# Optimization experiments

Measured on AMD Instinct MI355X. Metric: run time of the kernel, lower is better.

Reference implementation:

```python
import jax, jax.numpy as jnp
import numpy as np

B, T, C = 2, 2048, 2048
H = 16
D = C // H  # head_dim = 128


def rotate_half(x):
    x1, x2 = jnp.split(x, 2, axis=-1)
    return jnp.concatenate([-x2, x1], axis=-1)


def apply_rotary(q, k, cos, sin):
    # q,k: (B,H,T,D); cos,sin: (T,D/2)
    cos2 = jnp.concatenate([cos, cos], axis=-1)[None, None]  # (1,1,T,D)
    sin2 = jnp.concatenate([sin, sin], axis=-1)[None, None]
    return q * cos2 + rotate_half(q) * sin2, k * cos2 + rotate_half(k) * sin2


def setup_inputs() -> dict:
    key = jax.random.key(0)
    k1, k2, k3, k4 = jax.random.split(key, 4)
    x = jax.random.normal(k1, (B, T, C), dtype=jnp.float32)
    w_qkv = jax.random.normal(k2, (C, 3 * C), dtype=jnp.float32) * (C ** -0.5)
    w_out = jax.random.normal(k3, (C, C), dtype=jnp.float32) * (C ** -0.5)
    pos = jnp.arange(T, dtype=jnp.float32)[:, None]
    inv_freq = 1.0 / (10000.0 ** (jnp.arange(0, D, 2, dtype=jnp.float32) / D))  # (D/2,)
    ang = pos * inv_freq[None, :]  # (T, D/2)
    return {"x": x, "w_qkv": w_qkv, "w_out": w_out,
            "cos": jnp.cos(ang), "sin": jnp.sin(ang)}


def reference(x, w_qkv, w_out, cos, sin):
    b, t, c = x.shape
    qkv = x @ w_qkv  # (B,T,3C)
    qkv = qkv.reshape(b, t, 3, H, D)
    q, k, v = qkv[:, :, 0], qkv[:, :, 1], qkv[:, :, 2]  # (B,T,H,D)
    q = q.transpose(0, 2, 1, 3)  # (B,H,T,D)
    k = k.transpose(0, 2, 1, 3)
    v = v.transpose(0, 2, 1, 3)
    q, k = apply_rotary(q, k, cos, sin)
    scale = 1.0 / jnp.sqrt(jnp.asarray(D, dtype=x.dtype))
    scores = jnp.einsum('bhqd,bhkd->bhqk', q, k) * scale  # (B,H,T,T)
    causal = jnp.tril(jnp.ones((t, t), dtype=bool))
    scores = jnp.where(causal[None, None], scores, jnp.asarray(-jnp.inf, dtype=scores.dtype))
    attn = jax.nn.softmax(scores, axis=-1)
    out = jnp.einsum('bhqk,bhkd->bhqd', attn, v)  # (B,H,T,D)
    out = out.transpose(0, 2, 1, 3).reshape(b, t, c)
    return out @ w_out
```

## Files before the change

kernel.cpp:

```cpp
#include <hip/hip_runtime.h>


typedef __attribute__((ext_vector_type(8))) short short8;
typedef __attribute__((ext_vector_type(4))) float floatx4;
typedef __attribute__((ext_vector_type(4))) unsigned int uint4v;

#define MFMA16(a, b, c) __builtin_amdgcn_mfma_f32_16x16x32_bf16(a, b, c, 0, 0, 0)

__device__ inline unsigned short f2bf(float f) {
    union { float f; unsigned int i; } v; v.f = f;
    unsigned int r = v.i + 0x7fff + ((v.i >> 16) & 1);
    return (unsigned short)(r >> 16);
}

__device__ inline void gl2lds16(const unsigned short* g, unsigned short* l) {
    __builtin_amdgcn_global_load_lds(
        (const __attribute__((address_space(1))) unsigned int*)g,
        (__attribute__((address_space(3))) unsigned int*)l, 16, 0, 0);
}

__device__ __forceinline__ void bar_lds_only() {
    asm volatile("s_waitcnt lgkmcnt(0)" ::: "memory");
    __builtin_amdgcn_sched_barrier(0);
    __builtin_amdgcn_s_barrier();
    __builtin_amdgcn_sched_barrier(0);
}

__global__ __launch_bounds__(256) void cvt_k(const float* __restrict__ in,
                                             unsigned short* __restrict__ out, int n) {
    int i = (blockIdx.x * 256 + threadIdx.x) * 8;
    if (i + 7 < n) {
        float4 v0 = *(const float4*)(&in[i]);
        float4 v1 = *(const float4*)(&in[i + 4]);
        ushort4 o0, o1;
        o0.x = f2bf(v0.x); o0.y = f2bf(v0.y); o0.z = f2bf(v0.z); o0.w = f2bf(v0.w);
        o1.x = f2bf(v1.x); o1.y = f2bf(v1.y); o1.z = f2bf(v1.z); o1.w = f2bf(v1.w);
        *(ushort4*)(&out[i])     = o0;
        *(ushort4*)(&out[i + 4]) = o1;
    } else {
        for (int j = i; j < n; j++) out[j] = f2bf(in[j]);
    }
}

__global__ __launch_bounds__(256) void transpose_f2b_k(const float* __restrict__ in,
                                                       unsigned short* __restrict__ out,
                                                       int R, int Cc) {
    __shared__ unsigned short tile[32][33];
    int ct = blockIdx.x * 32;
    int rt = blockIdx.y * 32;
    int tx = threadIdx.x & 31;
    int ty = threadIdx.x >> 5;
#pragma unroll
    for (int i = 0; i < 32; i += 8)
        tile[ty + i][tx] = f2bf(in[(size_t)(rt + ty + i) * Cc + ct + tx]);
    __syncthreads();
#pragma unroll
    for (int i = 0; i < 32; i += 8)
        out[(size_t)(ct + ty + i) * R + rt + tx] = tile[tx][ty + i];
}

__global__ __launch_bounds__(256) void transpose_v_k(const unsigned short* __restrict__ qkv,
                                                     unsigned short* __restrict__ VT) {
    __shared__ unsigned short tile[32][33];
    int t0 = blockIdx.x * 32;
    int d0 = blockIdx.y * 32;
    int bh = blockIdx.z;
    int b = bh >> 4, h = bh & 15;
    int tx = threadIdx.x & 31;
    int ty = threadIdx.x >> 5;
#pragma unroll
    for (int i = 0; i < 32; i += 8)
        tile[ty + i][tx] =
            qkv[((size_t)(b * 2048 + t0 + ty + i) * 3 + 2) * 2048 + h * 128 + d0 + tx];
    __syncthreads();
#pragma unroll
    for (int i = 0; i < 32; i += 8)
        VT[((size_t)bh * 128 + d0 + ty + i) * 2048 + t0 + tx] = tile[tx][ty + i];
}

__global__ __launch_bounds__(256) void rotary_k(unsigned short* qkv,
                                                const float* __restrict__ cosT,
                                                const float* __restrict__ sinT) {
    int idx = blockIdx.x * 256 + threadIdx.x;
    int d    = idx & 63;
    int h    = (idx >> 6) & 15;
    int part = (idx >> 10) & 1;
    int t    = (idx >> 11) & 2047;
    int b    = idx >> 22;
    size_t base = ((size_t)(b * 2048 + t) * 3 + part) * 2048 + h * 128;
    float c = cosT[t * 64 + d];
    float s = sinT[t * 64 + d];
    union { unsigned int i; float f; } u1, u2;
    u1.i = ((unsigned int)qkv[base + d]) << 16;
    u2.i = ((unsigned int)qkv[base + d + 64]) << 16;
    float x1 = u1.f, x2 = u2.f;
    qkv[base + d]      = f2bf(x1 * c - x2 * s);
    qkv[base + d + 64] = f2bf(x2 * c + x1 * s);
}

template <bool OUTF32>
__global__ __launch_bounds__(256) void gemm_bt(const unsigned short* __restrict__ A, long lda,
                                               const unsigned short* __restrict__ Bt,
                                               void* __restrict__ Co, long ldc,
                                               int M, int N, int K) {
    __shared__ unsigned short a_lds[128 * 32];
    __shared__ unsigned short b_lds[128 * 32];
    int m0 = blockIdx.y * 128, n0 = blockIdx.x * 128;
    int tid = threadIdx.x;
    int lane = tid & 63, w = tid >> 6;
    int wm = (w >> 1) * 64, wn = (w & 1) * 64;
    int lr = lane & 15, quad = lane >> 4, lk = quad * 8;

    floatx4 acc[4][4];
    floatx4 zero4 = {0.f, 0.f, 0.f, 0.f};
#pragma unroll
    for (int i = 0; i < 4; i++)
#pragma unroll
        for (int j = 0; j < 4; j++) acc[i][j] = zero4;

    for (int k0 = 0; k0 < K; k0 += 32) {
#pragma unroll
        for (int i = 0; i < 2; i++) {
            int c = w * 128 + i * 64 + lane;
            int row = c >> 2, seg = (c & 3) * 8;
            gl2lds16(&A[(size_t)(m0 + row) * lda + k0 + seg], &a_lds[c * 8]);
            gl2lds16(&Bt[(size_t)(n0 + row) * K + k0 + seg], &b_lds[c * 8]);
        }
        __syncthreads();
        short8 af[4], bfr[4];
#pragma unroll
        for (int i = 0; i < 4; i++)
            af[i] = *(const short8*)(&a_lds[(wm + i * 16 + lr) * 32 + lk]);
#pragma unroll
        for (int j = 0; j < 4; j++)
            bfr[j] = *(const short8*)(&b_lds[(wn + j * 16 + lr) * 32 + lk]);
#pragma unroll
        for (int i = 0; i < 4; i++)
#pragma unroll
            for (int j = 0; j < 4; j++)
                acc[i][j] = MFMA16(af[i], bfr[j], acc[i][j]);
        __syncthreads();
    }
#pragma unroll
    for (int i = 0; i < 4; i++)
#pragma unroll
        for (int j = 0; j < 4; j++)
#pragma unroll
            for (int r = 0; r < 4; r++) {
                int row = m0 + wm + i * 16 + quad * 4 + r;
                int col = n0 + wn + j * 16 + lr;
                if (OUTF32)
                    ((float*)Co)[(size_t)row * ldc + col] = acc[i][j][r];
                else
                    ((unsigned short*)Co)[(size_t)row * ldc + col] = f2bf(acc[i][j][r]);
            }
}

__device__ __forceinline__ void attn_core(const short8 (&qf)[4], floatx4 (&o_acc)[8],
                                          float (&m_i)[4], float (&l_i)[4],
                                          const unsigned short* kb_lds,
                                          const unsigned short* vb_lds,
                                          unsigned short* p_w,
                                          int qrow0, int tk0, int lr, int quad, int lk) {
    floatx4 zero4 = {0.f, 0.f, 0.f, 0.f};
    const float scale = 0.08838834764831845f;

    floatx4 s[4];
#pragma unroll
    for (int n = 0; n < 4; n++) {
        s[n] = zero4;
#pragma unroll
        for (int c = 0; c < 4; c++) {
            short8 kb = *(const short8*)(
                &kb_lds[(n * 16 + lr) * 128 + (((c * 4 + quad) ^ lr) * 8)]);
            s[n] = MFMA16(qf[c], kb, s[n]);
        }
    }

    float rmax[4];
#pragma unroll
    for (int r = 0; r < 4; r++) {
        int tqr = qrow0 + quad * 4 + r;
        float mx = -1e30f;
#pragma unroll
        for (int n = 0; n < 4; n++) {
            int tk = tk0 + n * 16 + lr;
            float sv = s[n][r] * scale;
            sv = (tk > tqr) ? -1e30f : sv;
            s[n][r] = sv;
            mx = fmaxf(mx, sv);
        }
        rmax[r] = mx;
    }
#pragma unroll
    for (int off = 1; off < 16; off <<= 1)
#pragma unroll
        for (int r = 0; r < 4; r++)
            rmax[r] = fmaxf(rmax[r], __shfl_xor(rmax[r], off, 64));

    float alpha[4], rsum[4];
#pragma unroll
    for (int r = 0; r < 4; r++) {
        float mn = fmaxf(m_i[r], rmax[r]);
        alpha[r] = __expf(m_i[r] - mn);
        m_i[r] = mn;
        rsum[r] = 0.f;
    }
#pragma unroll
    for (int n = 0; n < 4; n++)
#pragma unroll
        for (int r = 0; r < 4; r++) {
            float p = __expf(s[n][r] - m_i[r]);
            rsum[r] += p;
            p_w[(quad * 4 + r) * 72 + n * 16 + lr] = f2bf(p);
        }
#pragma unroll
    for (int off = 1; off < 16; off <<= 1)
#pragma unroll
        for (int r = 0; r < 4; r++)
            rsum[r] += __shfl_xor(rsum[r], off, 64);
#pragma unroll
    for (int r = 0; r < 4; r++) l_i[r] = l_i[r] * alpha[r] + rsum[r];

#pragma unroll
    for (int dt = 0; dt < 8; dt++)
#pragma unroll
        for (int r = 0; r < 4; r++) o_acc[dt][r] *= alpha[r];

    short8 pa[2];
#pragma unroll
    for (int kc = 0; kc < 2; kc++)
        pa[kc] = *(const short8*)(&p_w[lr * 72 + kc * 32 + lk]);
#pragma unroll
    for (int dt = 0; dt < 8; dt++) {
#pragma unroll
        for (int kc = 0; kc < 2; kc++) {
            short8 vb = *(const short8*)(
                &vb_lds[(dt * 16 + lr) * 64 + (((kc * 4 + quad) ^ (lr & 7)) * 8)]);
            o_acc[dt] = MFMA16(pa[kc], vb, o_acc[dt]);
        }
    }
}

__global__ __launch_bounds__(512, 4) void attn_fast(unsigned short* qkv,
                                                    const unsigned short* __restrict__ VT) {
    const int T = 2048, Cc = 2048, Dd = 128;
    int xx = blockIdx.x;
    int qt = (xx & 1) ? (xx >> 1) : (15 - (xx >> 1));
    int bh = blockIdx.y;
    int b = bh >> 4, h = bh & 15;
    int tid = threadIdx.x, lane = tid & 63, w = tid >> 6;
    int lr = lane & 15, quad = lane >> 4, lk = quad * 8;
    int t0 = qt * 128;

    __shared__ __align__(16) unsigned short k_lds[64 * 128];
    __shared__ __align__(16) unsigned short v_lds[128 * 64];
    __shared__ __align__(16) unsigned short p_lds[8][16][72];

    short8 qf[4];
    {
        size_t qrow = (size_t)(b * T + t0 + w * 16 + lr) * 3 * Cc + h * Dd;
#pragma unroll
        for (int c = 0; c < 4; c++)
            qf[c] = *(const short8*)(&qkv[qrow + c * 32 + lk]);
    }

    floatx4 o_acc[8];
    floatx4 zero4 = {0.f, 0.f, 0.f, 0.f};
#pragma unroll
    for (int i = 0; i < 8; i++) o_acc[i] = zero4;
    float m_i[4], l_i[4];
#pragma unroll
    for (int r = 0; r < 4; r++) { m_i[r] = -1e30f; l_i[r] = 0.f; }

    int krow[2], kslot[2], vrow[2], vslot[2];
#pragma unroll
    for (int i = 0; i < 2; i++) {
        int c = i * 512 + tid;
        krow[i] = c >> 4; kslot[i] = c & 15;
        vrow[i] = c >> 3; vslot[i] = c & 7;
    }
    uint4v kA[2], vA[2];
    auto gload = [&](int kt) {
        int tk0 = kt * 64;
#pragma unroll
        for (int i = 0; i < 2; i++) {
            kA[i] = *(const uint4v*)(
                &qkv[((size_t)(b * T + tk0 + krow[i]) * 3 + 1) * Cc + h * Dd + kslot[i] * 8]);
            vA[i] = *(const uint4v*)(
                &VT[((size_t)bh * Dd + vrow[i]) * T + tk0 + vslot[i] * 8]);
        }
    };
    auto lwrite = [&]() {
#pragma unroll
        for (int i = 0; i < 2; i++) {
            *(uint4v*)(&k_lds[krow[i] * 128 + ((kslot[i] ^ (krow[i] & 15)) * 8)]) = kA[i];
            *(uint4v*)(&v_lds[vrow[i] * 64 + ((vslot[i] ^ (vrow[i] & 7)) * 8)]) = vA[i];
        }
    };

    int nkt = 2 * qt + 2;
    gload(0);

    for (int kt = 0; kt < nkt; kt++) {
        lwrite();
        bar_lds_only();
        if (kt + 1 < nkt) gload(kt + 1);
        int tk0 = kt * 64;
        if (tk0 <= t0 + w * 16 + 15)
            attn_core(qf, o_acc, m_i, l_i, k_lds, v_lds, &p_lds[w][0][0],
                      t0 + w * 16, tk0, lr, quad, lk);
        bar_lds_only();
    }

#pragma unroll
    for (int dt = 0; dt < 8; dt++)
#pragma unroll
        for (int r = 0; r < 4; r++) {
            int row = t0 + w * 16 + quad * 4 + r;
            int col = dt * 16 + lr;
            qkv[(size_t)(b * T + row) * 3 * Cc + h * Dd + col] = f2bf(o_acc[dt][r] * (1.0f / l_i[r]));
        }
}

extern "C" void kernel_launch(void* const* d_in, const int* in_sizes, int n_in,
                              void* d_out, int out_size, void* d_ws, size_t ws_size,
                              hipStream_t stream) {
    const float* x    = (const float*)d_in[0];
    const float* wqkv = (const float*)d_in[1];
    const float* wout = (const float*)d_in[2];
    const float* cosT = (const float*)d_in[3];
    const float* sinT = (const float*)d_in[4];
    float* out = (float*)d_out;

    unsigned short* qkv = (unsigned short*)d_ws;
    const size_t QKV = 25165824, XBF = 8388608;
    unsigned short* xbf = qkv + QKV;
    unsigned short* wTq = xbf + XBF;
    unsigned short* VT  = xbf;
    unsigned short* wTo = wTq;

    cvt_k<<<4096, 256, 0, stream>>>(x, xbf, 8388608);
    transpose_f2b_k<<<dim3(192, 64), 256, 0, stream>>>(wqkv, wTq, 2048, 6144);
    gemm_bt<false><<<dim3(48, 32), 256, 0, stream>>>(xbf, 2048, wTq, qkv, 6144,
                                                     4096, 6144, 2048);
    rotary_k<<<32768, 256, 0, stream>>>(qkv, cosT, sinT);
    transpose_f2b_k<<<dim3(64, 64), 256, 0, stream>>>(wout, wTo, 2048, 2048);
    transpose_v_k<<<dim3(64, 4, 32), 256, 0, stream>>>(qkv, VT);
    attn_fast<<<dim3(16, 32), 512, 0, stream>>>(qkv, VT);
    gemm_bt<true><<<dim3(16, 32), 256, 0, stream>>>(qkv, 6144, wTo, out, 2048,
                                                    4096, 2048, 2048);
}
```

Before: 501.8 us.

## Double-buffer GEMM LDS tiles and compute softmax row sums via MFMA ones column

The bf16 GEMM now keeps two LDS buffers for each operand. It issues the async global-to-LDS load of the next K tile before running the MFMAs on the current one, so the memory latency is hidden behind compute instead of stalling at a barrier every step. In the attention kernel, the per-row softmax denominator is no longer summed with cross-lane shuffles. It is accumulated by an extra MFMA against a row of bf16 ones stored after the V tile in LDS. This removes the shuffle reduction and uses the same bf16-rounded probabilities as the numerator, at the cost of double the GEMM LDS footprint and a small extra LDS row.

```diff
diff --git a/kernel.cpp b/kernel.cpp
--- a/kernel.cpp
+++ b/kernel.cpp
@@ -103,8 +103,8 @@
                                                const unsigned short* __restrict__ Bt,
                                                void* __restrict__ Co, long ldc,
                                                int M, int N, int K) {
-    __shared__ unsigned short a_lds[128 * 32];
-    __shared__ unsigned short b_lds[128 * 32];
+    __shared__ unsigned short a_lds[2][128 * 32];
+    __shared__ unsigned short b_lds[2][128 * 32];
     int m0 = blockIdx.y * 128, n0 = blockIdx.x * 128;
     int tid = threadIdx.x;
     int lane = tid & 63, w = tid >> 6;
@@ -118,22 +118,29 @@
 #pragma unroll
         for (int j = 0; j < 4; j++) acc[i][j] = zero4;
 
-    for (int k0 = 0; k0 < K; k0 += 32) {
+    auto stage = [&](int k0, int buf) {
 #pragma unroll
         for (int i = 0; i < 2; i++) {
             int c = w * 128 + i * 64 + lane;
             int row = c >> 2, seg = (c & 3) * 8;
-            gl2lds16(&A[(size_t)(m0 + row) * lda + k0 + seg], &a_lds[c * 8]);
-            gl2lds16(&Bt[(size_t)(n0 + row) * K + k0 + seg], &b_lds[c * 8]);
-        }
-        __syncthreads();
+            gl2lds16(&A[(size_t)(m0 + row) * lda + k0 + seg], &a_lds[buf][c * 8]);
+            gl2lds16(&Bt[(size_t)(n0 + row) * K + k0 + seg], &b_lds[buf][c * 8]);
+        }
+    };
+
+    int nt = K >> 5;
+    stage(0, 0);
+    __syncthreads();
+    for (int t = 0; t < nt; t++) {
+        int buf = t & 1;
+        if (t + 1 < nt) stage((t + 1) * 32, buf ^ 1);
         short8 af[4], bfr[4];
 #pragma unroll
         for (int i = 0; i < 4; i++)
-            af[i] = *(const short8*)(&a_lds[(wm + i * 16 + lr) * 32 + lk]);
+            af[i] = *(const short8*)(&a_lds[buf][(wm + i * 16 + lr) * 32 + lk]);
 #pragma unroll
         for (int j = 0; j < 4; j++)
-            bfr[j] = *(const short8*)(&b_lds[(wn + j * 16 + lr) * 32 + lk]);
+            bfr[j] = *(const short8*)(&b_lds[buf][(wn + j * 16 + lr) * 32 + lk]);
 #pragma unroll
         for (int i = 0; i < 4; i++)
 #pragma unroll
@@ -157,7 +164,8 @@
 }
 
 __device__ __forceinline__ void attn_core(const short8 (&qf)[4], floatx4 (&o_acc)[8],
-                                          float (&m_i)[4], float (&l_i)[4],
+                                          floatx4& o_l,
+                                          float (&m_i)[4],
                                           const unsigned short* kb_lds,
                                           const unsigned short* vb_lds,
                                           unsigned short* p_w,
@@ -198,34 +206,27 @@
         for (int r = 0; r < 4; r++)
             rmax[r] = fmaxf(rmax[r], __shfl_xor(rmax[r], off, 64));
 
-    float alpha[4], rsum[4];
+    float alpha[4];
 #pragma unroll
     for (int r = 0; r < 4; r++) {
         float mn = fmaxf(m_i[r], rmax[r]);
         alpha[r] = __expf(m_i[r] - mn);
         m_i[r] = mn;
-        rsum[r] = 0.f;
     }
 #pragma unroll
     for (int n = 0; n < 4; n++)
 #pragma unroll
         for (int r = 0; r < 4; r++) {
             float p = __expf(s[n][r] - m_i[r]);
-            rsum[r] += p;
             p_w[(quad * 4 + r) * 72 + n * 16 + lr] = f2bf(p);
         }
-#pragma unroll
-    for (int off = 1; off < 16; off <<= 1)
-#pragma unroll
-        for (int r = 0; r < 4; r++)
-            rsum[r] += __shfl_xor(rsum[r], off, 64);
-#pragma unroll
-    for (int r = 0; r < 4; r++) l_i[r] = l_i[r] * alpha[r] + rsum[r];
 
 #pragma unroll
     for (int dt = 0; dt < 8; dt++)
 #pragma unroll
         for (int r = 0; r < 4; r++) o_acc[dt][r] *= alpha[r];
+#pragma unroll
+    for (int r = 0; r < 4; r++) o_l[r] *= alpha[r];
 
     short8 pa[2];
 #pragma unroll
@@ -239,6 +240,11 @@
                 &vb_lds[(dt * 16 + lr) * 64 + (((kc * 4 + quad) ^ (lr & 7)) * 8)]);
             o_acc[dt] = MFMA16(pa[kc], vb, o_acc[dt]);
         }
+    }
+#pragma unroll
+    for (int kc = 0; kc < 2; kc++) {
+        short8 vb1 = *(const short8*)(&vb_lds[128 * 64 + (kc * 4 + quad) * 8]);
+        o_l = MFMA16(pa[kc], vb1, o_l);
     }
 }
 
@@ -254,8 +260,10 @@
     int t0 = qt * 128;
 
     __shared__ __align__(16) unsigned short k_lds[64 * 128];
-    __shared__ __align__(16) unsigned short v_lds[128 * 64];
+    __shared__ __align__(16) unsigned short v_lds[129 * 64];
     __shared__ __align__(16) unsigned short p_lds[8][16][72];
+
+    if (tid < 64) v_lds[128 * 64 + tid] = 0x3F80;
 
     short8 qf[4];
     {
@@ -269,9 +277,10 @@
     floatx4 zero4 = {0.f, 0.f, 0.f, 0.f};
 #pragma unroll
     for (int i = 0; i < 8; i++) o_acc[i] = zero4;
-    float m_i[4], l_i[4];
-#pragma unroll
-    for (int r = 0; r < 4; r++) { m_i[r] = -1e30f; l_i[r] = 0.f; }
+    floatx4 o_l = zero4;
+    float m_i[4];
+#pragma unroll
+    for (int r = 0; r < 4; r++) m_i[r] = -1e30f;
 
     int krow[2], kslot[2], vrow[2], vslot[2];
 #pragma unroll
@@ -308,7 +317,7 @@
         if (kt + 1 < nkt) gload(kt + 1);
         int tk0 = kt * 64;
         if (tk0 <= t0 + w * 16 + 15)
-            attn_core(qf, o_acc, m_i, l_i, k_lds, v_lds, &p_lds[w][0][0],
+            attn_core(qf, o_acc, o_l, m_i, k_lds, v_lds, &p_lds[w][0][0],
                       t0 + w * 16, tk0, lr, quad, lk);
         bar_lds_only();
     }
@@ -319,7 +328,7 @@
         for (int r = 0; r < 4; r++) {
             int row = t0 + w * 16 + quad * 4 + r;
             int col = dt * 16 + lr;
-            qkv[(size_t)(b * T + row) * 3 * Cc + h * Dd + col] = f2bf(o_acc[dt][r] * (1.0f / l_i[r]));
+            qkv[(size_t)(b * T + row) * 3 * Cc + h * Dd + col] = f2bf(o_acc[dt][r] * (1.0f / o_l[r]));
         }
 }
 
```

Result: faster. 454.6 us (-9.4%).
